# Optimization experiments

Hardware: AMD Instinct MI355X
Metric: run time of the kernel (lower is better)

Reference implementation:

```python
import jax, jax.numpy as jnp
import numpy as np

B, S, E, D, V, H, NL = 16, 1024, 64, 256, 10000, 8, 3
HD = D // H


def _ln(x, g, b):
    m = jnp.mean(x, -1, keepdims=True)
    v = jnp.mean((x - m) ** 2, -1, keepdims=True)
    return (x - m) / jnp.sqrt(v + 1e-5) * g + b


def _mha(q_in, kv_in, in_w, in_b, out_w, out_b, causal):
    # torch nn.MultiheadAttention with packed in_proj [3D, D]
    d = q_in.shape[-1]
    q = q_in @ in_w[:d].T + in_b[:d]
    k = kv_in @ in_w[d:2 * d].T + in_b[d:2 * d]
    v = kv_in @ in_w[2 * d:].T + in_b[2 * d:]
    sp = lambda t: t.reshape(t.shape[0], t.shape[1], H, HD).transpose(0, 2, 1, 3)
    q, k, v = sp(q), sp(k), sp(v)
    s = jnp.einsum('bhqd,bhkd->bhqk', q, k) / jnp.float32(np.sqrt(HD))
    if causal:
        L = s.shape[-1]
        s = jnp.where(jnp.tril(jnp.ones((L, L), bool)), s, jnp.float32(-1e30))
    a = jax.nn.softmax(s, -1)
    o = jnp.einsum('bhqk,bhkd->bhqd', a, v).transpose(0, 2, 1, 3).reshape(q_in.shape[0], -1, d)
    return o @ out_w.T + out_b


def setup_inputs() -> dict:
    key = jax.random.key(0)
    ks = iter(jax.random.split(key, 40))
    n = lambda *sh: jax.random.normal(next(ks), sh, jnp.float32) * 0.05
    d = dict(
        tractovka=n(B, E), context=n(B, E), card=n(B, E),
        enc_w=n(3, D, E), enc_b=n(3, D),
        enc_ln_g=jnp.ones((3, D), jnp.float32), enc_ln_b=jnp.zeros((3, D), jnp.float32),
        fusion_w=n(D, 3 * D), fusion_b=n(D),
        fusion_ln_g=jnp.ones(D, jnp.float32), fusion_ln_b=jnp.zeros(D, jnp.float32),
        tok_emb=n(V, D), pos_emb=n(1024, D),
        sa_in_w=n(NL, 3 * D, D), sa_in_b=n(NL, 3 * D), sa_out_w=n(NL, D, D), sa_out_b=n(NL, D),
        ca_in_w=n(NL, 3 * D, D), ca_in_b=n(NL, 3 * D), ca_out_w=n(NL, D, D), ca_out_b=n(NL, D),
        ln1_g=jnp.ones((NL, D), jnp.float32), ln1_b=jnp.zeros((NL, D), jnp.float32),
        ln2_g=jnp.ones((NL, D), jnp.float32), ln2_b=jnp.zeros((NL, D), jnp.float32),
        ln3_g=jnp.ones((NL, D), jnp.float32), ln3_b=jnp.zeros((NL, D), jnp.float32),
        ffn_w1=n(NL, 4 * D, D), ffn_b1=n(NL, 4 * D), ffn_w2=n(NL, D, 4 * D), ffn_b2=n(NL, D),
        out_w=n(V, D), out_b=n(V),
        prev_tokens=jax.random.randint(next(ks), (B, S), 0, V, jnp.int32),
    )
    return d


def reference(tractovka, context, card, enc_w, enc_b, enc_ln_g, enc_ln_b,
              fusion_w, fusion_b, fusion_ln_g, fusion_ln_b, tok_emb, pos_emb,
              sa_in_w, sa_in_b, sa_out_w, sa_out_b, ca_in_w, ca_in_b, ca_out_w, ca_out_b,
              ln1_g, ln1_b, ln2_g, ln2_b, ln3_g, ln3_b,
              ffn_w1, ffn_b1, ffn_w2, ffn_b2, out_w, out_b, prev_tokens):
    enc = lambda x, i: jax.nn.gelu(_ln(x @ enc_w[i].T + enc_b[i], enc_ln_g[i], enc_ln_b[i]), approximate=False)
    mem = jnp.concatenate([enc(tractovka, 0), enc(context, 1), enc(card, 2)], -1)
    mem = jax.nn.gelu(_ln(mem @ fusion_w.T + fusion_b, fusion_ln_g, fusion_ln_b), approximate=False)[:, None, :]  # [B,1,D]
    x = tok_emb[prev_tokens] + pos_emb[:prev_tokens.shape[1]][None]  # [B,S,D]
    for i in range(NL):  # post-norm decoder layer: self-attn, cross-attn, ReLU FFN
        x = _ln(x + _mha(x, x, sa_in_w[i], sa_in_b[i], sa_out_w[i], sa_out_b[i], True), ln1_g[i], ln1_b[i])
        x = _ln(x + _mha(x, mem, ca_in_w[i], ca_in_b[i], ca_out_w[i], ca_out_b[i], False), ln2_g[i], ln2_b[i])
        x = _ln(x + (jax.nn.relu(x @ ffn_w1[i].T + ffn_b1[i]) @ ffn_w2[i].T + ffn_b2[i]), ln3_g[i], ln3_b[i])
    return x @ out_w.T + out_b  # [B,S,V]
```

## Files before the change

kernel.cpp:

```cpp
#include <hip/hip_runtime.h>
#include <math.h>

constexpr int B = 16, S = 1024, D = 256, E = 64, H = 8, HD = 32;

typedef __attribute__((ext_vector_type(8))) short bf16x8;
typedef __attribute__((ext_vector_type(4))) float f32x4;

__device__ __forceinline__ float gelu_f(float x) {
  return 0.5f * x * (1.0f + erff(x * 0.70710678118654752440f));
}

__device__ __forceinline__ unsigned short f2bf(float f) {
  union { float f; unsigned u; } x; x.f = f;
  unsigned r = x.u + 0x7fff + ((x.u >> 16) & 1);
  return (unsigned short)(r >> 16);
}

__device__ __forceinline__ unsigned cvt_pk_bf16(float a, float b) {
  unsigned r;
  asm("v_cvt_pk_bf16_f32 %0, %1, %2" : "=v"(r) : "v"(a), "v"(b));
  return r;
}

__device__ __forceinline__ void gl16(const void* g, void* l) {
  __builtin_amdgcn_global_load_lds(
      (const __attribute__((address_space(1))) void*)g,
      (__attribute__((address_space(3))) void*)l, 16, 0, 0);
}

__global__ void k_cvt(const float* __restrict__ src, unsigned short* __restrict__ dst, int n) {
  int i = (blockIdx.x * 256 + threadIdx.x) * 4;
  if (i >= n) return;
  float4 v = *(const float4*)(src + i);
  dst[i + 0] = f2bf(v.x);
  dst[i + 1] = f2bf(v.y);
  dst[i + 2] = f2bf(v.z);
  dst[i + 3] = f2bf(v.w);
}

__global__ void k_embed(const int* __restrict__ tok,
                        const float* __restrict__ tok_emb,
                        const float* __restrict__ pos_emb,
                        float* __restrict__ x, unsigned short* __restrict__ xb) {
  int bs = blockIdx.x;
  int d = threadIdx.x;
  int s = bs & (S - 1);
  int t = tok[bs];
  float v = tok_emb[(size_t)t * D + d] + pos_emb[s * D + d];
  x[(size_t)bs * D + d] = v;
  xb[(size_t)bs * D + d] = f2bf(v);
}

__global__ void k_enc(const float* __restrict__ tr, const float* __restrict__ ctx,
                      const float* __restrict__ card,
                      const float* __restrict__ w, const float* __restrict__ bias,
                      const float* __restrict__ g, const float* __restrict__ bt,
                      float* __restrict__ cat) {
  int b = blockIdx.x, i = blockIdx.y, d = threadIdx.x;
  const float* xin = (i == 0 ? tr : (i == 1 ? ctx : card)) + b * E;
  const float* wr = w + ((size_t)i * D + d) * E;
  float acc = bias[i * D + d];
#pragma unroll 8
  for (int e = 0; e < E; ++e) acc += xin[e] * wr[e];
  __shared__ float s1[D], s2[D];
  s1[d] = acc; s2[d] = acc * acc;
  __syncthreads();
  for (int o = D / 2; o > 0; o >>= 1) {
    if (d < o) { s1[d] += s1[d + o]; s2[d] += s2[d + o]; }
    __syncthreads();
  }
  float mean = s1[0] * (1.0f / D);
  float var = s2[0] * (1.0f / D) - mean * mean;
  float nv = (acc - mean) * rsqrtf(var + 1e-5f) * g[i * D + d] + bt[i * D + d];
  cat[(size_t)b * (3 * D) + i * D + d] = gelu_f(nv);
}

__global__ void k_fusion(const float* __restrict__ cat, const float* __restrict__ w,
                         const float* __restrict__ bias, const float* __restrict__ g,
                         const float* __restrict__ bt, float* __restrict__ mem) {
  int b = blockIdx.x, d = threadIdx.x;
  const float* xr = cat + (size_t)b * (3 * D);
  const float* wr = w + (size_t)d * (3 * D);
  float acc = bias[d];
  for (int k = 0; k < 3 * D; ++k) acc += xr[k] * wr[k];
  __shared__ float s1[D], s2[D];
  s1[d] = acc; s2[d] = acc * acc;
  __syncthreads();
  for (int o = D / 2; o > 0; o >>= 1) {
    if (d < o) { s1[d] += s1[d + o]; s2[d] += s2[d + o]; }
    __syncthreads();
  }
  float mean = s1[0] * (1.0f / D);
  float var = s2[0] * (1.0f / D) - mean * mean;
  float nv = (acc - mean) * rsqrtf(var + 1e-5f) * g[d] + bt[d];
  mem[(size_t)b * D + d] = gelu_f(nv);
}

__global__ void k_ca(const float* __restrict__ mem,
                     const float* __restrict__ in_w, const float* __restrict__ in_b,
                     const float* __restrict__ out_w, const float* __restrict__ out_b,
                     float* __restrict__ ca_add) {
  int b = blockIdx.x, l = blockIdx.y, d = threadIdx.x;
  const float* mr = mem + (size_t)b * D;
  const float* wi = in_w + ((size_t)l * 3 * D + 2 * D + d) * D;
  float v = in_b[(size_t)l * 3 * D + 2 * D + d];
  for (int k = 0; k < D; ++k) v += mr[k] * wi[k];
  __shared__ float vs[D];
  vs[d] = v;
  __syncthreads();
  const float* wo = out_w + ((size_t)l * D + d) * D;
  float o = out_b[(size_t)l * D + d];
  for (int k = 0; k < D; ++k) o += vs[k] * wo[k];
  ca_add[((size_t)l * B + b) * D + d] = o;
}

__global__ __launch_bounds__(256)
void k_attn5(const unsigned short* __restrict__ qkv, unsigned short* __restrict__ out) {
  constexpr int KT = 64;
  __shared__ unsigned short Ks[2][KT * 32];
  __shared__ unsigned short Vt[2][32 * KT];
  __shared__ unsigned short Pl[4 * 32 * KT];

  const int t = threadIdx.x;
  const int w = t >> 6, lane = t & 63;
  const int lg = lane >> 4, lr = lane & 15;
  const int bh = blockIdx.y;
  const int h = bh & (H - 1), b = bh >> 3;
  const int qtile = (int)gridDim.x - 1 - (int)blockIdx.x;
  const int qb = qtile << 7;
  const int qw = qb + w * 32;
  const unsigned short* base = qkv + (size_t)b * S * 768 + h * HD;

  bf16x8 qf[2];
#pragma unroll
  for (int qr = 0; qr < 2; ++qr)
    qf[qr] = *(const bf16x8*)(base + (size_t)(qw + qr * 16 + lr) * 768 + lg * 8);

  f32x4 o[2][2];
#pragma unroll
  for (int qr = 0; qr < 2; ++qr)
#pragma unroll
    for (int dt = 0; dt < 2; ++dt) o[qr][dt] = (f32x4){0.f, 0.f, 0.f, 0.f};
  float mq[2], lq[2];
#pragma unroll
  for (int qr = 0; qr < 2; ++qr) { mq[qr] = -3.0e38f; lq[qr] = 0.f; }

  const float Cs = 0.17677669529663687f * 1.4426950408889634f;

  const int skey = t >> 2;
  const int sch = (t & 3) * 8;
  char* pbase = (char*)Pl + (w << 12);

  const int nkt = (qb + 128) >> 6;

  gl16(base + (size_t)skey * 768 + 256 + sch, (char*)Ks[0] + t * 16);
  bf16x8 vv = *(const bf16x8*)(base + (size_t)skey * 768 + 512 + sch);
  __syncthreads();

  for (int kti = 0; kti < nkt; ++kti) {
    const int kt = kti << 6;
    const int cur = kti & 1;

#pragma unroll
    for (int j = 0; j < 8; ++j) {
      int d = sch + j;
      int byteo = d * (KT * 2) + ((skey * 2) ^ ((d & 7) << 4));
      *(unsigned short*)((char*)Vt[cur] + byteo) = (unsigned short)vv[j];
    }
    if (kti + 1 < nkt) {
      const unsigned short* nb = base + (size_t)(kt + KT + skey) * 768;
      gl16(nb + 256 + sch, (char*)Ks[cur ^ 1] + t * 16);
      vv = *(const bf16x8*)(nb + 512 + sch);
    }

    const bool active = (kt <= qw + 31);
    if (active) {
      bf16x8 kf[4];
#pragma unroll
      for (int t4 = 0; t4 < 4; ++t4)
        kf[t4] = *(const bf16x8*)&Ks[cur][(t4 * 16 + lr) * 32 + lg * 8];
      f32x4 sc[2][4];
      __builtin_amdgcn_s_setprio(1);
#pragma unroll
      for (int qr = 0; qr < 2; ++qr)
#pragma unroll
        for (int t4 = 0; t4 < 4; ++t4)
          sc[qr][t4] = __builtin_amdgcn_mfma_f32_16x16x32_bf16(
              kf[t4], qf[qr], (f32x4){0.f, 0.f, 0.f, 0.f}, 0, 0, 0);
      __builtin_amdgcn_s_setprio(0);

      if (kt + KT > qw) {
#pragma unroll
        for (int qr = 0; qr < 2; ++qr) {
          int q = qw + qr * 16 + lr;
#pragma unroll
          for (int t4 = 0; t4 < 4; ++t4)
#pragma unroll
            for (int r = 0; r < 4; ++r) {
              int k = kt + t4 * 16 + lg * 4 + r;
              if (k > q) sc[qr][t4][r] = -3.0e38f;
            }
        }
      }

#pragma unroll
      for (int qr = 0; qr < 2; ++qr) {
        float mx = sc[qr][0][0];
#pragma unroll
        for (int t4 = 0; t4 < 4; ++t4)
#pragma unroll
          for (int r = 0; r < 4; ++r) mx = fmaxf(mx, sc[qr][t4][r]);
        mx = fmaxf(mx, __shfl_xor(mx, 16));
        mx = fmaxf(mx, __shfl_xor(mx, 32));
        mx = fmaxf(mx, mq[qr]);
        float cf = exp2f((mq[qr] - mx) * Cs);
        mq[qr] = mx;
        float nmxC = -mx * Cs;
        float ps = 0.f;
#pragma unroll
        for (int t4 = 0; t4 < 4; ++t4)
#pragma unroll
          for (int r = 0; r < 4; ++r) {
            float p = exp2f(fmaf(sc[qr][t4][r], Cs, nmxC));
            sc[qr][t4][r] = p;
            ps += p;
          }
        lq[qr] = lq[qr] * cf + ps;
#pragma unroll
        for (int r = 0; r < 4; ++r) {
          float cfo = __shfl(cf, (lane & 48) | (lg * 4 + r));
          o[qr][0][r] *= cfo;
          o[qr][1][r] *= cfo;
        }
        int ql = qr * 16 + lr;
        int swz = (ql & 7) << 4;
        char* prow = pbase + ql * (KT * 2);
#pragma unroll
        for (int t4 = 0; t4 < 4; ++t4) {
          unsigned lo = cvt_pk_bf16(sc[qr][t4][0], sc[qr][t4][1]);
          unsigned hi = cvt_pk_bf16(sc[qr][t4][2], sc[qr][t4][3]);
          *(uint2*)(prow + ((t4 * 32 + lg * 8) ^ swz)) = make_uint2(lo, hi);
        }
      }
    }

    __syncthreads();

    if (active) {
#pragma unroll
      for (int kp = 0; kp < 2; ++kp) {
        bf16x8 vf[2], pf[2];
        int kb = kp * 64 + lg * 16;
#pragma unroll
        for (int dt = 0; dt < 2; ++dt) {
          int d = dt * 16 + lr;
          vf[dt] = *(const bf16x8*)((char*)Vt[cur] + d * (KT * 2) + (kb ^ ((d & 7) << 4)));
        }
#pragma unroll
        for (int qr = 0; qr < 2; ++qr) {
          int ql = qr * 16 + lr;
          pf[qr] = *(const bf16x8*)(pbase + ql * (KT * 2) + (kb ^ ((ql & 7) << 4)));
        }
        __builtin_amdgcn_s_setprio(1);
#pragma unroll
        for (int qr = 0; qr < 2; ++qr)
#pragma unroll
          for (int dt = 0; dt < 2; ++dt)
            o[qr][dt] = __builtin_amdgcn_mfma_f32_16x16x32_bf16(
                pf[qr], vf[dt], o[qr][dt], 0, 0, 0);
        __builtin_amdgcn_s_setprio(0);
      }
    }
  }

#pragma unroll
  for (int qr = 0; qr < 2; ++qr) {
    float ls = lq[qr];
    ls += __shfl_xor(ls, 16);
    ls += __shfl_xor(ls, 32);
    float invq = 1.0f / ls;
#pragma unroll
    for (int r = 0; r < 4; ++r) {
      float inv = __shfl(invq, (lane & 48) | (lg * 4 + r));
      int q = qw + qr * 16 + lg * 4 + r;
      unsigned short* orow = out + (size_t)(b * S + q) * D + h * HD;
#pragma unroll
      for (int dt = 0; dt < 2; ++dt)
        orow[dt * 16 + lr] = f2bf(o[qr][dt][r] * inv);
    }
  }
}

template <int EPI, int OUTBF>
__global__ __launch_bounds__(256)
void k_gemm_mfma(const unsigned short* __restrict__ A,
                 const unsigned short* __restrict__ W,
                 const float* __restrict__ bias,
                 void* __restrict__ Cout,
                 int M, int N, int K) {
  __shared__ unsigned short As[128][32];
  __shared__ unsigned short Bs[128][32];
  int t = threadIdx.x;
  int row0 = blockIdx.y * 128, col0 = blockIdx.x * 128;
  int wid = t >> 6, lane = t & 63;
  int wr = wid >> 1, wc = wid & 1;
  int lrow = lane & 15, lko = (lane >> 4) * 8;

  f32x4 acc[4][4];
#pragma unroll
  for (int mi = 0; mi < 4; ++mi)
#pragma unroll
    for (int ni = 0; ni < 4; ++ni)
      acc[mi][ni] = (f32x4){0.f, 0.f, 0.f, 0.f};

  int c0 = t, c1 = t + 256;
  int ar0 = c0 >> 2, aq0 = (c0 & 3) * 8;
  int ar1 = c1 >> 2, aq1 = (c1 & 3) * 8;
  int wrow0 = col0 + ar0; if (wrow0 > N - 1) wrow0 = N - 1;
  int wrow1 = col0 + ar1; if (wrow1 > N - 1) wrow1 = N - 1;

  const unsigned short* A0 = A + (size_t)(row0 + ar0) * K + aq0;
  const unsigned short* A1 = A + (size_t)(row0 + ar1) * K + aq1;
  const unsigned short* W0 = W + (size_t)wrow0 * K + aq0;
  const unsigned short* W1 = W + (size_t)wrow1 * K + aq1;

  for (int kt = 0; kt < K; kt += 32) {
    gl16(A0 + kt, (char*)As + c0 * 16);
    gl16(A1 + kt, (char*)As + c1 * 16);
    gl16(W0 + kt, (char*)Bs + c0 * 16);
    gl16(W1 + kt, (char*)Bs + c1 * 16);
    __syncthreads();

    bf16x8 af[4], bfr[4];
#pragma unroll
    for (int mi = 0; mi < 4; ++mi)
      af[mi] = *(const bf16x8*)&As[wr * 64 + mi * 16 + lrow][lko];
#pragma unroll
    for (int ni = 0; ni < 4; ++ni)
      bfr[ni] = *(const bf16x8*)&Bs[wc * 64 + ni * 16 + lrow][lko];
#pragma unroll
    for (int mi = 0; mi < 4; ++mi)
#pragma unroll
      for (int ni = 0; ni < 4; ++ni)
        acc[mi][ni] = __builtin_amdgcn_mfma_f32_16x16x32_bf16(af[mi], bfr[ni], acc[mi][ni], 0, 0, 0);
    __syncthreads();
  }

  int rbase = row0 + wr * 64 + (lane >> 4) * 4;
  int cbase = col0 + wc * 64 + lrow;
#pragma unroll
  for (int ni = 0; ni < 4; ++ni) {
    int c = cbase + ni * 16;
    if (c < N) {
      float bv = bias[c];
#pragma unroll
      for (int mi = 0; mi < 4; ++mi) {
        int rr = rbase + mi * 16;
#pragma unroll
        for (int r = 0; r < 4; ++r) {
          float v = acc[mi][ni][r] + bv;
          if (EPI == 1) v = fmaxf(v, 0.0f);
          size_t off = (size_t)(rr + r) * N + c;
          if (OUTBF)
            ((unsigned short*)Cout)[off] = f2bf(v);
          else
            ((float*)Cout)[off] = v;
        }
      }
    }
  }
}

template <int NLN>
__global__ __launch_bounds__(256)
void k_gemm_ln(const unsigned short* __restrict__ A,
               const unsigned short* __restrict__ W,
               const float* __restrict__ bias,
               const float* __restrict__ res,
               const float* __restrict__ ca,
               const float* __restrict__ g1, const float* __restrict__ b1,
               const float* __restrict__ g2, const float* __restrict__ b2,
               float* __restrict__ xout, unsigned short* __restrict__ xb,
               int K) {
  __shared__ unsigned short As[64][32];
  __shared__ unsigned short Bs[256][32];
  __shared__ float red[2][64][4];
  int t = threadIdx.x;
  int row0 = blockIdx.x * 64;
  int wc = t >> 6, lane = t & 63;
  int lr = lane & 15, lg = lane >> 4;

  f32x4 acc[4][4];
#pragma unroll
  for (int mi = 0; mi < 4; ++mi)
#pragma unroll
    for (int ni = 0; ni < 4; ++ni)
      acc[mi][ni] = (f32x4){0.f, 0.f, 0.f, 0.f};

  const unsigned short* srcs[5];
  char* dsts[5];
#pragma unroll
  for (int i = 0; i < 5; ++i) {
    int c = t + (i << 8);
    if (c < 256) {
      int rw = c >> 2, q = (c & 3) * 8;
      srcs[i] = A + (size_t)(row0 + rw) * K + q;
      dsts[i] = (char*)As + c * 16;
    } else {
      int cb = c - 256;
      int rw = cb >> 2, q = (cb & 3) * 8;
      srcs[i] = W + (size_t)rw * K + q;
      dsts[i] = (char*)Bs + cb * 16;
    }
  }

  for (int kt = 0; kt < K; kt += 32) {
#pragma unroll
    for (int i = 0; i < 5; ++i) gl16(srcs[i] + kt, dsts[i]);
    __syncthreads();
    bf16x8 af[4], bfr[4];
#pragma unroll
    for (int mi = 0; mi < 4; ++mi)
      af[mi] = *(const bf16x8*)&As[mi * 16 + lr][lg * 8];
#pragma unroll
    for (int ni = 0; ni < 4; ++ni)
      bfr[ni] = *(const bf16x8*)&Bs[wc * 64 + ni * 16 + lr][lg * 8];
#pragma unroll
    for (int mi = 0; mi < 4; ++mi)
#pragma unroll
      for (int ni = 0; ni < 4; ++ni)
        acc[mi][ni] = __builtin_amdgcn_mfma_f32_16x16x32_bf16(af[mi], bfr[ni], acc[mi][ni], 0, 0, 0);
    __syncthreads();
  }

  int colb = wc * 64 + lr;
  float mean[4][4], rstd[4][4];

#pragma unroll
  for (int mi = 0; mi < 4; ++mi) {
#pragma unroll
    for (int r = 0; r < 4; ++r) {
      int rowl = mi * 16 + lg * 4 + r;
      int rowg = row0 + rowl;
      float s1 = 0.f, s2 = 0.f;
#pragma unroll
      for (int ni = 0; ni < 4; ++ni) {
        int c = colb + ni * 16;
        float v = acc[mi][ni][r] + bias[c] + res[(size_t)rowg * D + c];
        acc[mi][ni][r] = v;
        s1 += v; s2 += v * v;
      }
#pragma unroll
      for (int msk = 1; msk <= 8; msk <<= 1) {
        s1 += __shfl_xor(s1, msk);
        s2 += __shfl_xor(s2, msk);
      }
      if (lr == 0) { red[0][rowl][wc] = s1; red[1][rowl][wc] = s2; }
    }
  }
  __syncthreads();
#pragma unroll
  for (int mi = 0; mi < 4; ++mi)
#pragma unroll
    for (int r = 0; r < 4; ++r) {
      int rowl = mi * 16 + lg * 4 + r;
      f32x4 a = *(const f32x4*)&red[0][rowl][0];
      f32x4 bq = *(const f32x4*)&red[1][rowl][0];
      float s1 = a[0] + a[1] + a[2] + a[3];
      float s2 = bq[0] + bq[1] + bq[2] + bq[3];
      float mn = s1 * (1.0f / D);
      float vr = s2 * (1.0f / D) - mn * mn;
      mean[mi][r] = mn;
      rstd[mi][r] = rsqrtf(vr + 1e-5f);
    }
#pragma unroll
  for (int mi = 0; mi < 4; ++mi)
#pragma unroll
    for (int ni = 0; ni < 4; ++ni) {
      int c = colb + ni * 16;
      float gg = g1[c], bb = b1[c];
#pragma unroll
      for (int r = 0; r < 4; ++r)
        acc[mi][ni][r] = (acc[mi][ni][r] - mean[mi][r]) * rstd[mi][r] * gg + bb;
    }

  if (NLN == 2) {
    __syncthreads();
#pragma unroll
    for (int mi = 0; mi < 4; ++mi) {
#pragma unroll
      for (int r = 0; r < 4; ++r) {
        int rowl = mi * 16 + lg * 4 + r;
        int rowg = row0 + rowl;
        int bidx = rowg >> 10;
        float s1 = 0.f, s2 = 0.f;
#pragma unroll
        for (int ni = 0; ni < 4; ++ni) {
          int c = colb + ni * 16;
          float v = acc[mi][ni][r] + ca[(size_t)bidx * D + c];
          acc[mi][ni][r] = v;
          s1 += v; s2 += v * v;
        }
#pragma unroll
        for (int msk = 1; msk <= 8; msk <<= 1) {
          s1 += __shfl_xor(s1, msk);
          s2 += __shfl_xor(s2, msk);
        }
        if (lr == 0) { red[0][rowl][wc] = s1; red[1][rowl][wc] = s2; }
      }
    }
    __syncthreads();
#pragma unroll
    for (int mi = 0; mi < 4; ++mi)
#pragma unroll
      for (int r = 0; r < 4; ++r) {
        int rowl = mi * 16 + lg * 4 + r;
        f32x4 a = *(const f32x4*)&red[0][rowl][0];
        f32x4 bq = *(const f32x4*)&red[1][rowl][0];
        float s1 = a[0] + a[1] + a[2] + a[3];
        float s2 = bq[0] + bq[1] + bq[2] + bq[3];
        float mn = s1 * (1.0f / D);
        float vr = s2 * (1.0f / D) - mn * mn;
        mean[mi][r] = mn;
        rstd[mi][r] = rsqrtf(vr + 1e-5f);
      }
#pragma unroll
    for (int mi = 0; mi < 4; ++mi)
#pragma unroll
      for (int ni = 0; ni < 4; ++ni) {
        int c = colb + ni * 16;
        float gg = g2[c], bb = b2[c];
#pragma unroll
        for (int r = 0; r < 4; ++r)
          acc[mi][ni][r] = (acc[mi][ni][r] - mean[mi][r]) * rstd[mi][r] * gg + bb;
      }
  }

#pragma unroll
  for (int mi = 0; mi < 4; ++mi)
#pragma unroll
    for (int r = 0; r < 4; ++r) {
      int rowg = row0 + mi * 16 + lg * 4 + r;
#pragma unroll
      for (int ni = 0; ni < 4; ++ni) {
        int c = colb + ni * 16;
        float v = acc[mi][ni][r];
        xout[(size_t)rowg * D + c] = v;
        xb[(size_t)rowg * D + c] = f2bf(v);
      }
    }
}

extern "C" void kernel_launch(void* const* d_in, const int* in_sizes, int n_in,
                              void* d_out, int out_size, void* d_ws, size_t ws_size,
                              hipStream_t stream) {
  (void)in_sizes; (void)n_in; (void)out_size; (void)ws_size;
  const float* tractovka = (const float*)d_in[0];
  const float* context   = (const float*)d_in[1];
  const float* card      = (const float*)d_in[2];
  const float* enc_w     = (const float*)d_in[3];
  const float* enc_b     = (const float*)d_in[4];
  const float* enc_ln_g  = (const float*)d_in[5];
  const float* enc_ln_b  = (const float*)d_in[6];
  const float* fusion_w  = (const float*)d_in[7];
  const float* fusion_b  = (const float*)d_in[8];
  const float* fusion_ln_g = (const float*)d_in[9];
  const float* fusion_ln_b = (const float*)d_in[10];
  const float* tok_emb   = (const float*)d_in[11];
  const float* pos_emb   = (const float*)d_in[12];
  const float* sa_in_w   = (const float*)d_in[13];
  const float* sa_in_b   = (const float*)d_in[14];
  const float* sa_out_w  = (const float*)d_in[15];
  const float* sa_out_b  = (const float*)d_in[16];
  const float* ca_in_w   = (const float*)d_in[17];
  const float* ca_in_b   = (const float*)d_in[18];
  const float* ca_out_w  = (const float*)d_in[19];
  const float* ca_out_b  = (const float*)d_in[20];
  const float* ln1_g     = (const float*)d_in[21];
  const float* ln1_b     = (const float*)d_in[22];
  const float* ln2_g     = (const float*)d_in[23];
  const float* ln2_b     = (const float*)d_in[24];
  const float* ln3_g     = (const float*)d_in[25];
  const float* ln3_b     = (const float*)d_in[26];
  const float* ffn_w1    = (const float*)d_in[27];
  const float* ffn_b1    = (const float*)d_in[28];
  const float* ffn_w2    = (const float*)d_in[29];
  const float* ffn_b2    = (const float*)d_in[30];
  const float* out_w     = (const float*)d_in[31];
  const float* out_b     = (const float*)d_in[32];
  const int*   prev      = (const int*)d_in[33];
  float* out = (float*)d_out;

  const int M = B * S;

  float* ws = (float*)d_ws;
  float* x      = ws;
  float* bufA   = x + (size_t)M * D;
  float* bufB   = bufA + (size_t)M * 768;
  float* cat    = bufB + (size_t)M * D;
  float* mem    = cat + (size_t)B * 3 * D;
  float* ca_add = mem + (size_t)B * D;
  unsigned short* xb    = (unsigned short*)(ca_add + (size_t)3 * B * D);
  unsigned short* attnb = xb + (size_t)M * D;
  unsigned short* wbf   = attnb + (size_t)M * D;
  unsigned short* qkvb  = (unsigned short*)bufA;
  unsigned short* ffn1b = (unsigned short*)bufA;

  const int n_qkvw = 3 * 768 * D;
  const int n_outw = 3 * D * D;
  const int n_f1w  = 3 * 1024 * D;
  const int n_f2w  = 3 * D * 1024;
  const int n_vw   = 10000 * D;
  unsigned short* w_qkv = wbf;
  unsigned short* w_out = w_qkv + n_qkvw;
  unsigned short* w_f1  = w_out + n_outw;
  unsigned short* w_f2  = w_f1 + n_f1w;
  unsigned short* w_v   = w_f2 + n_f2w;

  k_cvt<<<(n_qkvw / 4 + 255) / 256, 256, 0, stream>>>(sa_in_w, w_qkv, n_qkvw);
  k_cvt<<<(n_outw / 4 + 255) / 256, 256, 0, stream>>>(sa_out_w, w_out, n_outw);
  k_cvt<<<(n_f1w / 4 + 255) / 256, 256, 0, stream>>>(ffn_w1, w_f1, n_f1w);
  k_cvt<<<(n_f2w / 4 + 255) / 256, 256, 0, stream>>>(ffn_w2, w_f2, n_f2w);
  k_cvt<<<(n_vw / 4 + 255) / 256, 256, 0, stream>>>(out_w, w_v, n_vw);

  k_embed<<<M, D, 0, stream>>>(prev, tok_emb, pos_emb, x, xb);
  k_enc<<<dim3(B, 3), D, 0, stream>>>(tractovka, context, card, enc_w, enc_b,
                                      enc_ln_g, enc_ln_b, cat);
  k_fusion<<<B, D, 0, stream>>>(cat, fusion_w, fusion_b, fusion_ln_g, fusion_ln_b, mem);
  k_ca<<<dim3(B, 3), D, 0, stream>>>(mem, ca_in_w, ca_in_b, ca_out_w, ca_out_b, ca_add);

  for (int l = 0; l < 3; ++l) {
    k_gemm_mfma<0, 1><<<dim3(6, M / 128), 256, 0, stream>>>(
        xb, w_qkv + (size_t)l * 768 * D, sa_in_b + (size_t)l * 3 * D, qkvb,
        M, 768, D);
    k_attn5<<<dim3(S / 128, B * H), 256, 0, stream>>>(qkvb, attnb);
    k_gemm_ln<2><<<dim3(M / 64), 256, 0, stream>>>(
        attnb, w_out + (size_t)l * D * D, sa_out_b + (size_t)l * D,
        x, ca_add + (size_t)l * B * D,
        ln1_g + (size_t)l * D, ln1_b + (size_t)l * D,
        ln2_g + (size_t)l * D, ln2_b + (size_t)l * D,
        x, xb, D);
    k_gemm_mfma<1, 1><<<dim3(8, M / 128), 256, 0, stream>>>(
        xb, w_f1 + (size_t)l * 1024 * D, ffn_b1 + (size_t)l * 4 * D, ffn1b,
        M, 1024, D);
    k_gemm_ln<1><<<dim3(M / 64), 256, 0, stream>>>(
        ffn1b, w_f2 + (size_t)l * D * 1024, ffn_b2 + (size_t)l * D,
        x, nullptr,
        ln3_g + (size_t)l * D, ln3_b + (size_t)l * D,
        nullptr, nullptr,
        x, xb, 1024);
  }
  k_gemm_mfma<0, 0><<<dim3(79, M / 128), 256, 0, stream>>>(
      xb, w_v, out_b, out, M, 10000, D);
}
```

Measured before the change: 877.4 us.

## Widen attention blocks, lazily rescale softmax, double-buffer GEMM-LN tiles

Attention now runs 512-thread blocks that each cover 256 queries. This halves how often each head's K/V tiles are reloaded, and the V loads are split across more threads. The online softmax only rescales O and l when some row max grows by more than a threshold, which skips the exp and shuffle work on most tiles. This relies on the bounded growth of exp2 to stay numerically safe. Separately, the GEMM+LayerNorm kernel double-buffers its A and B LDS tiles so the next loads overlap the MFMA work, and it raises wave priority around the MFMAs.

```diff
diff --git a/kernel.cpp b/kernel.cpp
--- a/kernel.cpp
+++ b/kernel.cpp
@@ -4,6 +4,7 @@
 constexpr int B = 16, S = 1024, D = 256, E = 64, H = 8, HD = 32;
 
 typedef __attribute__((ext_vector_type(8))) short bf16x8;
+typedef __attribute__((ext_vector_type(4))) short bf16x4;
 typedef __attribute__((ext_vector_type(4))) float f32x4;
 
 __device__ __forceinline__ float gelu_f(float x) {
@@ -114,12 +115,12 @@
   ca_add[((size_t)l * B + b) * D + d] = o;
 }
 
-__global__ __launch_bounds__(256)
-void k_attn5(const unsigned short* __restrict__ qkv, unsigned short* __restrict__ out) {
+__global__ __launch_bounds__(512)
+void k_attn6(const unsigned short* __restrict__ qkv, unsigned short* __restrict__ out) {
   constexpr int KT = 64;
   __shared__ unsigned short Ks[2][KT * 32];
   __shared__ unsigned short Vt[2][32 * KT];
-  __shared__ unsigned short Pl[4 * 32 * KT];
+  __shared__ unsigned short Pl[8 * 32 * KT];
 
   const int t = threadIdx.x;
   const int w = t >> 6, lane = t & 63;
@@ -127,7 +128,7 @@
   const int bh = blockIdx.y;
   const int h = bh & (H - 1), b = bh >> 3;
   const int qtile = (int)gridDim.x - 1 - (int)blockIdx.x;
-  const int qb = qtile << 7;
+  const int qb = qtile << 8;
   const int qw = qb + w * 32;
   const unsigned short* base = qkv + (size_t)b * S * 768 + h * HD;
 
@@ -149,12 +150,14 @@
 
   const int skey = t >> 2;
   const int sch = (t & 3) * 8;
+  const int vkey = t >> 3;
+  const int vch = (t & 7) * 4;
   char* pbase = (char*)Pl + (w << 12);
 
-  const int nkt = (qb + 128) >> 6;
-
-  gl16(base + (size_t)skey * 768 + 256 + sch, (char*)Ks[0] + t * 16);
-  bf16x8 vv = *(const bf16x8*)(base + (size_t)skey * 768 + 512 + sch);
+  const int nkt = (qb + 256) >> 6;
+
+  if (t < 256) gl16(base + (size_t)skey * 768 + 256 + sch, (char*)Ks[0] + t * 16);
+  bf16x4 vv = *(const bf16x4*)(base + (size_t)vkey * 768 + 512 + vch);
   __syncthreads();
 
   for (int kti = 0; kti < nkt; ++kti) {
@@ -162,15 +165,15 @@
     const int cur = kti & 1;
 
 #pragma unroll
-    for (int j = 0; j < 8; ++j) {
-      int d = sch + j;
-      int byteo = d * (KT * 2) + ((skey * 2) ^ ((d & 7) << 4));
+    for (int j = 0; j < 4; ++j) {
+      int d = vch + j;
+      int byteo = d * (KT * 2) + ((vkey * 2) ^ ((d & 7) << 4));
       *(unsigned short*)((char*)Vt[cur] + byteo) = (unsigned short)vv[j];
     }
     if (kti + 1 < nkt) {
-      const unsigned short* nb = base + (size_t)(kt + KT + skey) * 768;
-      gl16(nb + 256 + sch, (char*)Ks[cur ^ 1] + t * 16);
-      vv = *(const bf16x8*)(nb + 512 + sch);
+      if (t < 256)
+        gl16(base + (size_t)(kt + KT + skey) * 768 + 256 + sch, (char*)Ks[cur ^ 1] + t * 16);
+      vv = *(const bf16x4*)(base + (size_t)(kt + KT + vkey) * 768 + 512 + vch);
     }
 
     const bool active = (kt <= qw + 31);
@@ -212,10 +215,19 @@
           for (int r = 0; r < 4; ++r) mx = fmaxf(mx, sc[qr][t4][r]);
         mx = fmaxf(mx, __shfl_xor(mx, 16));
         mx = fmaxf(mx, __shfl_xor(mx, 32));
-        mx = fmaxf(mx, mq[qr]);
-        float cf = exp2f((mq[qr] - mx) * Cs);
-        mq[qr] = mx;
-        float nmxC = -mx * Cs;
+        if (__any(mx > mq[qr] + 8.0f)) {
+          float mn = fmaxf(mx, mq[qr]);
+          float cf = exp2f((mq[qr] - mn) * Cs);
+          mq[qr] = mn;
+          lq[qr] *= cf;
+#pragma unroll
+          for (int r = 0; r < 4; ++r) {
+            float cfo = __shfl(cf, (lane & 48) | (lg * 4 + r));
+            o[qr][0][r] *= cfo;
+            o[qr][1][r] *= cfo;
+          }
+        }
+        float nmxC = -mq[qr] * Cs;
         float ps = 0.f;
 #pragma unroll
         for (int t4 = 0; t4 < 4; ++t4)
@@ -225,13 +237,7 @@
             sc[qr][t4][r] = p;
             ps += p;
           }
-        lq[qr] = lq[qr] * cf + ps;
-#pragma unroll
-        for (int r = 0; r < 4; ++r) {
-          float cfo = __shfl(cf, (lane & 48) | (lg * 4 + r));
-          o[qr][0][r] *= cfo;
-          o[qr][1][r] *= cfo;
-        }
+        lq[qr] += ps;
         int ql = qr * 16 + lr;
         int swz = (ql & 7) << 4;
         char* prow = pbase + ql * (KT * 2);
@@ -382,8 +388,8 @@
                const float* __restrict__ g2, const float* __restrict__ b2,
                float* __restrict__ xout, unsigned short* __restrict__ xb,
                int K) {
-  __shared__ unsigned short As[64][32];
-  __shared__ unsigned short Bs[256][32];
+  __shared__ unsigned short As[2][64][32];
+  __shared__ unsigned short Bs[2][256][32];
   __shared__ float red[2][64][4];
   int t = threadIdx.x;
   int row0 = blockIdx.x * 64;
@@ -398,38 +404,50 @@
       acc[mi][ni] = (f32x4){0.f, 0.f, 0.f, 0.f};
 
   const unsigned short* srcs[5];
-  char* dsts[5];
+  char* dsts[2][5];
 #pragma unroll
   for (int i = 0; i < 5; ++i) {
     int c = t + (i << 8);
     if (c < 256) {
       int rw = c >> 2, q = (c & 3) * 8;
       srcs[i] = A + (size_t)(row0 + rw) * K + q;
-      dsts[i] = (char*)As + c * 16;
+      dsts[0][i] = (char*)As[0] + c * 16;
+      dsts[1][i] = (char*)As[1] + c * 16;
     } else {
       int cb = c - 256;
       int rw = cb >> 2, q = (cb & 3) * 8;
       srcs[i] = W + (size_t)rw * K + q;
-      dsts[i] = (char*)Bs + cb * 16;
-    }
-  }
-
-  for (int kt = 0; kt < K; kt += 32) {
-#pragma unroll
-    for (int i = 0; i < 5; ++i) gl16(srcs[i] + kt, dsts[i]);
-    __syncthreads();
+      dsts[0][i] = (char*)Bs[0] + cb * 16;
+      dsts[1][i] = (char*)Bs[1] + cb * 16;
+    }
+  }
+
+  const int nsteps = K >> 5;
+#pragma unroll
+  for (int i = 0; i < 5; ++i) gl16(srcs[i], dsts[0][i]);
+  __syncthreads();
+
+  for (int s = 0; s < nsteps; ++s) {
+    const int cur = s & 1;
+    if (s + 1 < nsteps) {
+      int off = (s + 1) << 5;
+#pragma unroll
+      for (int i = 0; i < 5; ++i) gl16(srcs[i] + off, dsts[cur ^ 1][i]);
+    }
     bf16x8 af[4], bfr[4];
 #pragma unroll
     for (int mi = 0; mi < 4; ++mi)
-      af[mi] = *(const bf16x8*)&As[mi * 16 + lr][lg * 8];
+      af[mi] = *(const bf16x8*)&As[cur][mi * 16 + lr][lg * 8];
 #pragma unroll
     for (int ni = 0; ni < 4; ++ni)
-      bfr[ni] = *(const bf16x8*)&Bs[wc * 64 + ni * 16 + lr][lg * 8];
+      bfr[ni] = *(const bf16x8*)&Bs[cur][wc * 64 + ni * 16 + lr][lg * 8];
+    __builtin_amdgcn_s_setprio(1);
 #pragma unroll
     for (int mi = 0; mi < 4; ++mi)
 #pragma unroll
       for (int ni = 0; ni < 4; ++ni)
         acc[mi][ni] = __builtin_amdgcn_mfma_f32_16x16x32_bf16(af[mi], bfr[ni], acc[mi][ni], 0, 0, 0);
+    __builtin_amdgcn_s_setprio(0);
     __syncthreads();
   }
 
@@ -633,7 +651,7 @@
     k_gemm_mfma<0, 1><<<dim3(6, M / 128), 256, 0, stream>>>(
         xb, w_qkv + (size_t)l * 768 * D, sa_in_b + (size_t)l * 3 * D, qkvb,
         M, 768, D);
-    k_attn5<<<dim3(S / 128, B * H), 256, 0, stream>>>(qkvb, attnb);
+    k_attn6<<<dim3(S / 256, B * H), 512, 0, stream>>>(qkvb, attnb);
     k_gemm_ln<2><<<dim3(M / 64), 256, 0, stream>>>(
         attnb, w_out + (size_t)l * D * D, sa_out_b + (size_t)l * D,
         x, ca_add + (size_t)l * B * D,
```

Measured after the change: 816.3 us. 1.07x faster.
